# Performance work log

Hardware: AMD Instinct MI355X
Metric: run time of the kernel (lower is better)

The kernel has to match this reference:

```python
import jax, jax.numpy as jnp
import numpy as np

# ---- static config (matches init_kwargs) ----
B, S, E = 1, 2048, 2048
H, G, D = 32, 8, 64            # query heads, kv groups, head_dim
GS = H // G                    # group size = 4
SW = 128                       # sliding window
LAYER_IDX = 0                  # even -> sliding-window mask active
ROPE_BASE = 10000.0
ORIG_CTX = 4096.0              # yarn_original_context_length
YARN_SCALE = 2.0               # yarn_scaling_factor
BETA_FAST, BETA_SLOW = 32.0, 1.0


def _rope_sincos(position_ids):
    # YaRN-adjusted RoPE angles, computed directly at position_ids.
    freqs = 1.0 / ROPE_BASE ** (jnp.arange(0, D, 2, dtype=jnp.float32) / D)  # [D/2]
    wave_len = 2.0 * jnp.pi / freqs
    low = ORIG_CTX / BETA_FAST
    high = ORIG_CTX / BETA_SLOW
    t = jnp.clip((wave_len - low) / (high - low), 0.0, 1.0)
    eff = freqs * (1.0 - t) + (freqs / YARN_SCALE) * t
    conc = 0.1 * jnp.log(jnp.float32(YARN_SCALE)) + 1.0
    ang = position_ids[..., None].astype(jnp.float32) * eff * conc           # [B,S,D/2]
    ang = jnp.concatenate([ang, ang], axis=-1)                               # [B,S,D]
    # add head axis for broadcast over [B,H,S,D]
    return jnp.sin(ang)[:, None], jnp.cos(ang)[:, None]


def _apply_rope(x, sin, cos):
    x1, x2 = x[..., : D // 2], x[..., D // 2 :]
    rotated = jnp.concatenate([-x2, x1], axis=-1)
    return x * cos + rotated * sin


def setup_inputs() -> dict:
    key = jax.random.key(0)
    ks = jax.random.split(key, 6)
    x = jax.random.normal(ks[0], (B, S, E), dtype=jnp.float32)
    position_ids = jnp.broadcast_to(jnp.arange(S, dtype=jnp.int32), (B, S))
    # additive causal mask: -inf above the diagonal
    i = jnp.arange(S)[:, None]
    j = jnp.arange(S)[None, :]
    attn_mask = jnp.where(j > i, -jnp.inf, 0.0).astype(jnp.float32)[None, None]  # [1,1,S,S]
    sc = 0.02
    Wqkv = jax.random.normal(ks[1], ((H + 2 * G) * D, E), dtype=jnp.float32) * sc
    bqkv = jax.random.normal(ks[2], ((H + 2 * G) * D,), dtype=jnp.float32) * sc
    Wout = jax.random.normal(ks[3], (E, H * D), dtype=jnp.float32) * sc
    bout = jax.random.normal(ks[4], (E,), dtype=jnp.float32) * sc
    sinks = jax.random.normal(ks[5], (1, H, 1, 1), dtype=jnp.float32)
    return {"x": x, "position_ids": position_ids, "attn_mask": attn_mask,
            "Wqkv": Wqkv, "bqkv": bqkv, "Wout": Wout, "bout": bout, "sinks": sinks}


def reference(x, position_ids, attn_mask, Wqkv, bqkv, Wout, bout, sinks):
    b, s, _ = x.shape
    qkv = (x @ Wqkv.T + bqkv).reshape(b, s, H + 2 * G, D)
    Q = qkv[:, :, :H].transpose(0, 2, 1, 3)              # [B,H,S,D]
    K = qkv[:, :, H : H + G].transpose(0, 2, 1, 3)       # [B,G,S,D]
    V = qkv[:, :, H + G :].transpose(0, 2, 1, 3)         # [B,G,S,D]

    sin, cos = _rope_sincos(position_ids)
    Q = _apply_rope(Q, sin, cos)
    K = _apply_rope(K, sin, cos)

    # GQA: group query heads, no K/V duplication
    Qg = Q.reshape(b, G, GS, s, D)
    scores = jnp.einsum("bgmqd,bgkd->bgmqk", Qg, K) / (D ** 0.5)  # [B,G,GS,S,S]
    scores = scores.reshape(b, H, s, s) + attn_mask

    # sliding-window mask (layer_idx even, kv_len > sliding_window)
    if LAYER_IDX % 2 == 0 and s > SW:
        i = jnp.arange(s)[:, None]
        j = jnp.arange(s)[None, :]
        scores = jnp.where(j <= i - SW, -jnp.inf, scores)

    # learned sink logit prepended before softmax, then dropped
    sink = jnp.broadcast_to(sinks, (b, H, s, 1))
    attn = jax.nn.softmax(jnp.concatenate([sink, scores], axis=-1), axis=-1)[..., 1:]

    ctx = jnp.einsum("bgmqk,bgkd->bgmqd", attn.reshape(b, G, GS, s, s), V)
    ctx = ctx.reshape(b, H, s, D).transpose(0, 2, 1, 3).reshape(b, s, H * D)
    return ctx @ Wout.T + bout
```

## Files before the change

### kernel.cpp

```cpp
#include <hip/hip_runtime.h>
#include <cstdint>

#define S_LEN 2048
#define EMB   2048
#define NHEAD 32
#define NKV   8
#define HDIM  64
#define NQKV  3072

typedef __attribute__((ext_vector_type(8))) short bf16x8;
typedef __attribute__((ext_vector_type(4))) float f32x4;

__device__ __forceinline__ unsigned short f2bf(float f){
  union { float f; unsigned int u; } v; v.f = f;
  unsigned int r = v.u + 0x7FFFu + ((v.u >> 16) & 1u);
  return (unsigned short)(r >> 16);
}
__device__ __forceinline__ float bf2f(unsigned short u){
  union { unsigned int u; float f; } v; v.u = ((unsigned int)u) << 16;
  return v.f;
}

__global__ void cvt_bf16_kernel(const float* __restrict__ in,
                                unsigned short* __restrict__ out, int n4){
  int i = blockIdx.x * 256 + threadIdx.x;
  if (i < n4){
    const float4 v = ((const float4*)in)[i];
    ushort4 o;
    o.x = f2bf(v.x); o.y = f2bf(v.y); o.z = f2bf(v.z); o.w = f2bf(v.w);
    ((ushort4*)out)[i] = o;
  }
}

template<int OUT_BF16>
__global__ __launch_bounds__(256) void gemm_bt(const unsigned short* __restrict__ A,
                                               const unsigned short* __restrict__ B,
                                               const float* __restrict__ bias,
                                               void* __restrict__ Cout,
                                               int M, int N, int K){
  __shared__ unsigned short As[128*32];
  __shared__ unsigned short Bs[128*32];
  const int tid  = threadIdx.x;
  const int lane = tid & 63;
  const int wid  = tid >> 6;
  const int m0 = blockIdx.y * 128;
  const int n0 = blockIdx.x * 128;
  const int wm = (wid >> 1) * 64;
  const int wn = (wid & 1) * 64;
  const int fm = lane & 15;
  const int q8 = (lane >> 4) * 8;

  f32x4 acc[4][4];
#pragma unroll
  for (int i = 0; i < 4; ++i)
#pragma unroll
    for (int j = 0; j < 4; ++j) acc[i][j] = {0.f, 0.f, 0.f, 0.f};

  const int srow = lane >> 2;
  const int scol = (lane & 3) * 8;
  const unsigned short* Ag = A + (size_t)(m0 + wid*32 + srow) * K + scol;
  const unsigned short* Bg = B + (size_t)(n0 + wid*32 + srow) * K + scol;
  unsigned short* AsW = &As[(wid*32)*32];
  unsigned short* BsW = &Bs[(wid*32)*32];

  for (int k0 = 0; k0 < K; k0 += 32){
    __syncthreads();
    __builtin_amdgcn_global_load_lds((const __attribute__((address_space(1))) void*)(Ag + k0),
        (__attribute__((address_space(3))) void*)AsW, 16, 0, 0);
    __builtin_amdgcn_global_load_lds((const __attribute__((address_space(1))) void*)(Ag + k0 + (size_t)16*K),
        (__attribute__((address_space(3))) void*)(AsW + 16*32), 16, 0, 0);
    __builtin_amdgcn_global_load_lds((const __attribute__((address_space(1))) void*)(Bg + k0),
        (__attribute__((address_space(3))) void*)BsW, 16, 0, 0);
    __builtin_amdgcn_global_load_lds((const __attribute__((address_space(1))) void*)(Bg + k0 + (size_t)16*K),
        (__attribute__((address_space(3))) void*)(BsW + 16*32), 16, 0, 0);
    __syncthreads();

    bf16x8 af[4], bfr[4];
#pragma unroll
    for (int i = 0; i < 4; ++i) af[i]  = *(const bf16x8*)&As[(wm + i*16 + fm)*32 + q8];
#pragma unroll
    for (int j = 0; j < 4; ++j) bfr[j] = *(const bf16x8*)&Bs[(wn + j*16 + fm)*32 + q8];
#pragma unroll
    for (int i = 0; i < 4; ++i)
#pragma unroll
      for (int j = 0; j < 4; ++j)
        acc[i][j] = __builtin_amdgcn_mfma_f32_16x16x32_bf16(af[i], bfr[j], acc[i][j], 0, 0, 0);
  }

  const int quad = lane >> 4;
#pragma unroll
  for (int j = 0; j < 4; ++j){
    const int col = n0 + wn + j*16 + fm;
    const float bv = bias[col];
#pragma unroll
    for (int i = 0; i < 4; ++i){
#pragma unroll
      for (int r = 0; r < 4; ++r){
        const int row = m0 + wm + i*16 + quad*4 + r;
        const float v = acc[i][j][r] + bv;
        if (OUT_BF16) ((unsigned short*)Cout)[(size_t)row*N + col] = f2bf(v);
        else          ((float*)Cout)[(size_t)row*N + col] = v;
      }
    }
  }
}

__global__ __launch_bounds__(256) void rope_kernel(unsigned short* __restrict__ qkv,
                                                   const int* __restrict__ pos){
  const int s = blockIdx.x;
  const float ps = (float)pos[s];
  unsigned short* p = qkv + (size_t)s * NQKV;
  for (int e = threadIdx.x; e < 40*64; e += 256){
    const int head = e >> 6, d = e & 63;
    const int i = d & 31;
    const float freq = __expf(-(float)i * (9.210340371976184f / 32.0f));
    const float wl = 6.283185307179586f / freq;
    float t = (wl - 128.0f) * (1.0f / 3968.0f);
    t = fminf(fmaxf(t, 0.f), 1.f);
    const float eff = freq * (1.0f - 0.5f * t);
    const float ang = ps * eff * 1.0693147180559945f;
    const float c = cosf(ang), sn = sinf(ang);
    const int ch = (head < NHEAD) ? head*HDIM + d : EMB + (head - NHEAD)*HDIM + d;
    const float x  = bf2f(p[ch]);
    const float ot = (d < 32) ? bf2f(p[ch + 32]) : bf2f(p[ch - 32]);
    p[ch] = f2bf((d < 32) ? (x * c - ot * sn) : (x * c + ot * sn));
  }
}

__global__ __launch_bounds__(256) void attn_kernel(const unsigned short* __restrict__ qkv,
                                                   const float* __restrict__ sinks,
                                                   unsigned short* __restrict__ ctxb){
  const int h  = blockIdx.y;
  const int q0 = blockIdx.x * 64;
  const int g  = h >> 2;
  const int tid  = threadIdx.x;
  const int lane = tid & 63;
  const int wid  = tid >> 6;
  const int fm   = lane & 15;
  const int quad = lane >> 4;

  __shared__ unsigned short Ks[2*64*40];
  __shared__ unsigned short Vt[2*64*34];
  __shared__ unsigned short Pl[4*2*16*40];

  const int qrow = q0 + wid*16 + fm;
  bf16x8 aq[2];
#pragma unroll
  for (int ks = 0; ks < 2; ++ks)
    aq[ks] = *(const bf16x8*)(qkv + (size_t)qrow*NQKV + h*HDIM + ks*32 + quad*8);

  f32x4 o[4];
#pragma unroll
  for (int nt = 0; nt < 4; ++nt) o[nt] = {0.f, 0.f, 0.f, 0.f};
  float m_[4], l_[4];
#pragma unroll
  for (int r = 0; r < 4; ++r){ m_[r] = -30000.f; l_[r] = 0.f; }

  const int qbase = q0 + wid*16 + quad*4;
  int cs0 = q0 - 128; if (cs0 < 0) cs0 = 0;

  unsigned short* plw = &Pl[wid*1280];

  for (int cs = cs0; cs <= q0; cs += 64){
    __syncthreads();
#pragma unroll
    for (int it = 0; it < 2; ++it){
      const int e = (tid + it*256) * 8;
      const int key = e >> 6, d0 = e & 63;
      const unsigned short* kp = qkv + (size_t)(cs + key)*NQKV + EMB + g*HDIM + d0;
      *(bf16x8*)&Ks[(d0>>5)*2560 + key*40 + (d0 & 31)] = *(const bf16x8*)kp;
      const bf16x8 vv = *(const bf16x8*)(kp + NKV*HDIM);
      const unsigned short* vs = (const unsigned short*)&vv;
      unsigned short* vt = &Vt[(key>>5)*2176 + (key & 31)];
#pragma unroll
      for (int j = 0; j < 8; ++j) vt[(d0 + j)*34] = vs[j];
    }
    __syncthreads();

    f32x4 sa[4];
#pragma unroll
    for (int nt = 0; nt < 4; ++nt){
      sa[nt] = {0.f, 0.f, 0.f, 0.f};
#pragma unroll
      for (int ks = 0; ks < 2; ++ks){
        const bf16x8 bk = *(const bf16x8*)&Ks[ks*2560 + (nt*16 + fm)*40 + quad*8];
        sa[nt] = __builtin_amdgcn_mfma_f32_16x16x32_bf16(aq[ks], bk, sa[nt], 0, 0, 0);
      }
    }

#pragma unroll
    for (int nt = 0; nt < 4; ++nt){
      const int key = cs + nt*16 + fm;
#pragma unroll
      for (int r = 0; r < 4; ++r){
        const float s = sa[nt][r] * 0.125f;
        const bool ok = (unsigned)(qbase + r - key) < 128u;
        sa[nt][r] = ok ? s : -1e30f;
      }
    }

#pragma unroll
    for (int r = 0; r < 4; ++r){
      float t = fmaxf(fmaxf(sa[0][r], sa[1][r]), fmaxf(sa[2][r], sa[3][r]));
#pragma unroll
      for (int off = 1; off < 16; off <<= 1) t = fmaxf(t, __shfl_xor(t, off, 64));
      const float nm = fmaxf(m_[r], t);
      const float al = __expf(m_[r] - nm);
#pragma unroll
      for (int nt = 0; nt < 4; ++nt) sa[nt][r] = __expf(sa[nt][r] - nm);
      float ts = (sa[0][r] + sa[1][r]) + (sa[2][r] + sa[3][r]);
#pragma unroll
      for (int off = 1; off < 16; off <<= 1) ts += __shfl_xor(ts, off, 64);
      l_[r] = l_[r]*al + ts;
      m_[r] = nm;
#pragma unroll
      for (int nt = 0; nt < 4; ++nt) o[nt][r] *= al;
    }

#pragma unroll
    for (int nt = 0; nt < 4; ++nt)
#pragma unroll
      for (int r = 0; r < 4; ++r)
        plw[(nt>>1)*640 + (quad*4 + r)*40 + (nt&1)*16 + fm] = f2bf(sa[nt][r]);
    __asm__ volatile("s_waitcnt lgkmcnt(0)" ::: "memory");

    bf16x8 pa[2];
#pragma unroll
    for (int ks = 0; ks < 2; ++ks)
      pa[ks] = *(const bf16x8*)&plw[ks*640 + fm*40 + quad*8];
    const unsigned int* vb = (const unsigned int*)Vt;
#pragma unroll
    for (int nt = 0; nt < 4; ++nt){
#pragma unroll
      for (int ks = 0; ks < 2; ++ks){
        const int ui = ks*1088 + (nt*16 + fm)*17 + quad*4;
        union { unsigned int u[4]; bf16x8 v; } bb;
        bb.u[0] = vb[ui+0]; bb.u[1] = vb[ui+1]; bb.u[2] = vb[ui+2]; bb.u[3] = vb[ui+3];
        o[nt] = __builtin_amdgcn_mfma_f32_16x16x32_bf16(pa[ks], bb.v, o[nt], 0, 0, 0);
      }
    }
  }

  const float snk = sinks[h];
#pragma unroll
  for (int r = 0; r < 4; ++r){
    const float nm = fmaxf(m_[r], snk);
    const float e  = __expf(m_[r] - nm);
    const float denom = l_[r]*e + __expf(snk - nm);
    const float sc = e / denom;
    const size_t row = (size_t)(qbase + r)*EMB + h*HDIM;
#pragma unroll
    for (int nt = 0; nt < 4; ++nt)
      ctxb[row + nt*16 + fm] = f2bf(o[nt][r] * sc);
  }
}

extern "C" void kernel_launch(void* const* d_in, const int* in_sizes, int n_in,
                              void* d_out, int out_size, void* d_ws, size_t ws_size,
                              hipStream_t stream){
  const float* x     = (const float*)d_in[0];
  const int*   pos   = (const int*)  d_in[1];
  const float* Wqkv  = (const float*)d_in[3];
  const float* bqkv  = (const float*)d_in[4];
  const float* Wout  = (const float*)d_in[5];
  const float* bout  = (const float*)d_in[6];
  const float* sinks = (const float*)d_in[7];

  char* ws = (char*)d_ws;
  unsigned short* xb   = (unsigned short*)(ws);
  unsigned short* wqb  = (unsigned short*)(ws + 8388608);
  unsigned short* wob  = (unsigned short*)(ws + 20971520);
  unsigned short* qkv  = (unsigned short*)(ws + 29360128);
  unsigned short* ctxb = (unsigned short*)(ws + 41943040);

  cvt_bf16_kernel<<<dim3(4096), dim3(256), 0, stream>>>(x,    xb,  1048576);
  cvt_bf16_kernel<<<dim3(6144), dim3(256), 0, stream>>>(Wqkv, wqb, 1572864);
  cvt_bf16_kernel<<<dim3(4096), dim3(256), 0, stream>>>(Wout, wob, 1048576);

  gemm_bt<1><<<dim3(24, 16), dim3(256), 0, stream>>>(xb, wqb, bqkv, (void*)qkv, 2048, 3072, 2048);
  rope_kernel<<<dim3(2048), dim3(256), 0, stream>>>(qkv, pos);
  attn_kernel<<<dim3(32, 32), dim3(256), 0, stream>>>(qkv, sinks, ctxb);
  gemm_bt<0><<<dim3(16, 16), dim3(256), 0, stream>>>(ctxb, wob, bout, d_out, 2048, 2048, 2048);
}
```

Measured before the change: 241.4 us.

## Fuse RoPE into QKV GEMM epilogue, merge conversions, halve GEMM M-tile

Drops the standalone RoPE kernel and applies the rotation in the QKV GEMM epilogue. Each wave holds 64 columns, which is one full head, so the rotate-half partner sits in the same thread's registers. The three fp32-to-bf16 conversion launches become one kernel that picks its source by index range. The GEMM M-tile shrinks from 128 to 64 rows, doubling the block count for better CU occupancy, at the cost of less B-tile reuse per block. RoPE now uses the fast __sincosf intrinsic, which may lose precision at large angles.

```diff
diff --git a/kernel.cpp b/kernel.cpp
--- a/kernel.cpp
+++ b/kernel.cpp
@@ -21,109 +21,135 @@
   return v.f;
 }
 
-__global__ void cvt_bf16_kernel(const float* __restrict__ in,
-                                unsigned short* __restrict__ out, int n4){
+__global__ __launch_bounds__(256) void cvt3_kernel(const float* __restrict__ a, unsigned short* __restrict__ da, int na,
+                                                   const float* __restrict__ b, unsigned short* __restrict__ db, int nb,
+                                                   const float* __restrict__ c, unsigned short* __restrict__ dc, int nc){
   int i = blockIdx.x * 256 + threadIdx.x;
-  if (i < n4){
-    const float4 v = ((const float4*)in)[i];
-    ushort4 o;
-    o.x = f2bf(v.x); o.y = f2bf(v.y); o.z = f2bf(v.z); o.w = f2bf(v.w);
-    ((ushort4*)out)[i] = o;
-  }
-}
-
-template<int OUT_BF16>
+  const float* s; unsigned short* d;
+  if (i < na){ s = a; d = da; }
+  else if (i < na + nb){ s = b; d = db; i -= na; }
+  else if (i < na + nb + nc){ s = c; d = dc; i -= na + nb; }
+  else return;
+  const float4 v = ((const float4*)s)[i];
+  ushort4 o;
+  o.x = f2bf(v.x); o.y = f2bf(v.y); o.z = f2bf(v.z); o.w = f2bf(v.w);
+  ((ushort4*)d)[i] = o;
+}
+
+template<int OUT_BF16, int ROPE>
 __global__ __launch_bounds__(256) void gemm_bt(const unsigned short* __restrict__ A,
                                                const unsigned short* __restrict__ B,
                                                const float* __restrict__ bias,
                                                void* __restrict__ Cout,
+                                               const int* __restrict__ pos,
                                                int M, int N, int K){
-  __shared__ unsigned short As[128*32];
+  __shared__ unsigned short As[64*32];
   __shared__ unsigned short Bs[128*32];
   const int tid  = threadIdx.x;
   const int lane = tid & 63;
   const int wid  = tid >> 6;
-  const int m0 = blockIdx.y * 128;
+  const int m0 = blockIdx.y * 64;
   const int n0 = blockIdx.x * 128;
-  const int wm = (wid >> 1) * 64;
+  const int wm = (wid >> 1) * 32;
   const int wn = (wid & 1) * 64;
   const int fm = lane & 15;
   const int q8 = (lane >> 4) * 8;
-
-  f32x4 acc[4][4];
-#pragma unroll
-  for (int i = 0; i < 4; ++i)
+  const int quad = lane >> 4;
+
+  f32x4 acc[2][4];
+#pragma unroll
+  for (int i = 0; i < 2; ++i)
 #pragma unroll
     for (int j = 0; j < 4; ++j) acc[i][j] = {0.f, 0.f, 0.f, 0.f};
 
   const int srow = lane >> 2;
   const int scol = (lane & 3) * 8;
-  const unsigned short* Ag = A + (size_t)(m0 + wid*32 + srow) * K + scol;
+  const unsigned short* Ag = A + (size_t)(m0 + wid*16 + srow) * K + scol;
   const unsigned short* Bg = B + (size_t)(n0 + wid*32 + srow) * K + scol;
-  unsigned short* AsW = &As[(wid*32)*32];
+  unsigned short* AsW = &As[(wid*16)*32];
   unsigned short* BsW = &Bs[(wid*32)*32];
 
   for (int k0 = 0; k0 < K; k0 += 32){
     __syncthreads();
     __builtin_amdgcn_global_load_lds((const __attribute__((address_space(1))) void*)(Ag + k0),
         (__attribute__((address_space(3))) void*)AsW, 16, 0, 0);
-    __builtin_amdgcn_global_load_lds((const __attribute__((address_space(1))) void*)(Ag + k0 + (size_t)16*K),
-        (__attribute__((address_space(3))) void*)(AsW + 16*32), 16, 0, 0);
     __builtin_amdgcn_global_load_lds((const __attribute__((address_space(1))) void*)(Bg + k0),
         (__attribute__((address_space(3))) void*)BsW, 16, 0, 0);
     __builtin_amdgcn_global_load_lds((const __attribute__((address_space(1))) void*)(Bg + k0 + (size_t)16*K),
         (__attribute__((address_space(3))) void*)(BsW + 16*32), 16, 0, 0);
     __syncthreads();
 
-    bf16x8 af[4], bfr[4];
-#pragma unroll
-    for (int i = 0; i < 4; ++i) af[i]  = *(const bf16x8*)&As[(wm + i*16 + fm)*32 + q8];
+    bf16x8 af[2], bfr[4];
+#pragma unroll
+    for (int i = 0; i < 2; ++i) af[i]  = *(const bf16x8*)&As[(wm + i*16 + fm)*32 + q8];
 #pragma unroll
     for (int j = 0; j < 4; ++j) bfr[j] = *(const bf16x8*)&Bs[(wn + j*16 + fm)*32 + q8];
 #pragma unroll
-    for (int i = 0; i < 4; ++i)
+    for (int i = 0; i < 2; ++i)
 #pragma unroll
       for (int j = 0; j < 4; ++j)
         acc[i][j] = __builtin_amdgcn_mfma_f32_16x16x32_bf16(af[i], bfr[j], acc[i][j], 0, 0, 0);
   }
 
-  const int quad = lane >> 4;
+  float v[2][4][4];
+#pragma unroll
+  for (int j = 0; j < 4; ++j){
+    const float bv = bias[n0 + wn + j*16 + fm];
+#pragma unroll
+    for (int i = 0; i < 2; ++i)
+#pragma unroll
+      for (int r = 0; r < 4; ++r) v[i][j][r] = acc[i][j][r] + bv;
+  }
+
+  if (ROPE && (n0 + wn) < 2560){
+    float cc[2][4][2], ss[2][4][2];
+#pragma unroll
+    for (int jp = 0; jp < 2; ++jp){
+      const float ifr = (float)(jp*16 + fm);
+      const float freq = __expf(-ifr * (9.210340371976184f / 32.0f));
+      const float wl = 6.283185307179586f / freq;
+      float t = fminf(fmaxf((wl - 128.0f) * (1.0f / 3968.0f), 0.f), 1.f);
+      const float eff = freq * (1.0f - 0.5f * t) * 1.0693147180559945f;
+#pragma unroll
+      for (int i = 0; i < 2; ++i)
+#pragma unroll
+        for (int r = 0; r < 4; ++r){
+          const int row = m0 + wm + i*16 + quad*4 + r;
+          const float ang = (float)pos[row] * eff;
+          __sincosf(ang, &ss[i][r][jp], &cc[i][r][jp]);
+        }
+    }
+    float o[2][4][4];
+#pragma unroll
+    for (int i = 0; i < 2; ++i)
+#pragma unroll
+      for (int j = 0; j < 4; ++j){
+        const int jp = j & 1;
+        const float sgn = (j < 2) ? -1.f : 1.f;
+#pragma unroll
+        for (int r = 0; r < 4; ++r)
+          o[i][j][r] = v[i][j][r]*cc[i][r][jp] + sgn*v[i][j^2][r]*ss[i][r][jp];
+      }
+#pragma unroll
+    for (int i = 0; i < 2; ++i)
+#pragma unroll
+      for (int j = 0; j < 4; ++j)
+#pragma unroll
+        for (int r = 0; r < 4; ++r) v[i][j][r] = o[i][j][r];
+  }
+
 #pragma unroll
   for (int j = 0; j < 4; ++j){
     const int col = n0 + wn + j*16 + fm;
-    const float bv = bias[col];
-#pragma unroll
-    for (int i = 0; i < 4; ++i){
+#pragma unroll
+    for (int i = 0; i < 2; ++i){
 #pragma unroll
       for (int r = 0; r < 4; ++r){
         const int row = m0 + wm + i*16 + quad*4 + r;
-        const float v = acc[i][j][r] + bv;
-        if (OUT_BF16) ((unsigned short*)Cout)[(size_t)row*N + col] = f2bf(v);
-        else          ((float*)Cout)[(size_t)row*N + col] = v;
-      }
-    }
-  }
-}
-
-__global__ __launch_bounds__(256) void rope_kernel(unsigned short* __restrict__ qkv,
-                                                   const int* __restrict__ pos){
-  const int s = blockIdx.x;
-  const float ps = (float)pos[s];
-  unsigned short* p = qkv + (size_t)s * NQKV;
-  for (int e = threadIdx.x; e < 40*64; e += 256){
-    const int head = e >> 6, d = e & 63;
-    const int i = d & 31;
-    const float freq = __expf(-(float)i * (9.210340371976184f / 32.0f));
-    const float wl = 6.283185307179586f / freq;
-    float t = (wl - 128.0f) * (1.0f / 3968.0f);
-    t = fminf(fmaxf(t, 0.f), 1.f);
-    const float eff = freq * (1.0f - 0.5f * t);
-    const float ang = ps * eff * 1.0693147180559945f;
-    const float c = cosf(ang), sn = sinf(ang);
-    const int ch = (head < NHEAD) ? head*HDIM + d : EMB + (head - NHEAD)*HDIM + d;
-    const float x  = bf2f(p[ch]);
-    const float ot = (d < 32) ? bf2f(p[ch + 32]) : bf2f(p[ch - 32]);
-    p[ch] = f2bf((d < 32) ? (x * c - ot * sn) : (x * c + ot * sn));
+        if (OUT_BF16) ((unsigned short*)Cout)[(size_t)row*N + col] = f2bf(v[i][j][r]);
+        else          ((float*)Cout)[(size_t)row*N + col] = v[i][j][r];
+      }
+    }
   }
 }
 
@@ -158,7 +184,6 @@
 
   const int qbase = q0 + wid*16 + quad*4;
   int cs0 = q0 - 128; if (cs0 < 0) cs0 = 0;
-
   unsigned short* plw = &Pl[wid*1280];
 
   for (int cs = cs0; cs <= q0; cs += 64){
@@ -273,12 +298,11 @@
   unsigned short* qkv  = (unsigned short*)(ws + 29360128);
   unsigned short* ctxb = (unsigned short*)(ws + 41943040);
 
-  cvt_bf16_kernel<<<dim3(4096), dim3(256), 0, stream>>>(x,    xb,  1048576);
-  cvt_bf16_kernel<<<dim3(6144), dim3(256), 0, stream>>>(Wqkv, wqb, 1572864);
-  cvt_bf16_kernel<<<dim3(4096), dim3(256), 0, stream>>>(Wout, wob, 1048576);
-
-  gemm_bt<1><<<dim3(24, 16), dim3(256), 0, stream>>>(xb, wqb, bqkv, (void*)qkv, 2048, 3072, 2048);
-  rope_kernel<<<dim3(2048), dim3(256), 0, stream>>>(qkv, pos);
+  cvt3_kernel<<<dim3(14336), dim3(256), 0, stream>>>(x, xb, 1048576,
+                                                     Wqkv, wqb, 1572864,
+                                                     Wout, wob, 1048576);
+
+  gemm_bt<1,1><<<dim3(24, 32), dim3(256), 0, stream>>>(xb, wqb, bqkv, (void*)qkv, pos, 2048, 3072, 2048);
   attn_kernel<<<dim3(32, 32), dim3(256), 0, stream>>>(qkv, sinks, ctxb);
-  gemm_bt<0><<<dim3(16, 16), dim3(256), 0, stream>>>(ctxb, wob, bout, d_out, 2048, 2048, 2048);
-}
+  gemm_bt<0,0><<<dim3(16, 32), dim3(256), 0, stream>>>(ctxb, wob, bout, d_out, nullptr, 2048, 2048, 2048);
+}
```

After: 214.5 us. 1.13x faster.
